# Kernel tuning notes

Measured on AMD Instinct MI355X. Metric: run time of the kernel, lower is better.

Reference implementation:

```python
import jax, jax.numpy as jnp
import numpy as np

N_NODES = 100000
N_EDGES = 1600000
N_GRAPHS = 64
F = 50
N_LAYERS = 3
EPS_STD = 1e-5
EPS_BN = 1e-5


def _glorot(key, shape):
    fan_in, fan_out = shape[0], shape[1]
    lim = float(np.sqrt(6.0 / (fan_in + fan_out)))
    return jax.random.uniform(key, shape, jnp.float32, -lim, lim)


def setup_inputs() -> dict:
    key = jax.random.key(0)
    ks = jax.random.split(key, 20)
    x = jax.random.normal(ks[0], (N_NODES, 2), jnp.float32)
    edge_index = jax.random.randint(ks[1], (2, N_EDGES), 0, N_NODES, jnp.int32)
    batch_ids = jnp.sort(jax.random.randint(ks[2], (N_NODES,), 0, N_GRAPHS, jnp.int32))
    inp = {
        "x": x,
        "edge_index": edge_index,
        "batch_ids": batch_ids,
        "W_gcn": _glorot(ks[3], (2, F)),
        "b_gcn": jnp.zeros((F,), jnp.float32),
        # stacked per-layer PNA params [L, ...]
        "pre_W": jnp.stack([_glorot(jax.random.fold_in(ks[4], i), (2 * F, F)) for i in range(N_LAYERS)]),
        "pre_b": jnp.zeros((N_LAYERS, F), jnp.float32),
        "post_W": jnp.stack([_glorot(jax.random.fold_in(ks[5], i), (13 * F, F)) for i in range(N_LAYERS)]),
        "post_b": jnp.zeros((N_LAYERS, F), jnp.float32),
        "lin_W": jnp.stack([_glorot(jax.random.fold_in(ks[6], i), (F, F)) for i in range(N_LAYERS)]),
        "lin_b": jnp.zeros((N_LAYERS, F), jnp.float32),
        "bn_gamma": jnp.ones((N_LAYERS, F), jnp.float32),
        "bn_beta": jnp.zeros((N_LAYERS, F), jnp.float32),
        "mlp_W1": _glorot(ks[7], (F, 25)),
        "mlp_b1": jnp.zeros((25,), jnp.float32),
        "mlp_W2": _glorot(ks[8], (25, 1)),
        "mlp_b2": jnp.zeros((1,), jnp.float32),
    }
    return inp


def _pna_layer(x, src, dst, deg_raw, deg_c, avg_log, Wp, bp, Wq, bq, Wl, bl):
    # pre-NN on messages: concat(x_i, x_j) -> F   (i = target/dst, j = source/src)
    h = jnp.concatenate([x[dst], x[src]], axis=-1) @ Wp + bp  # [E, F]
    dc = deg_c[:, None]
    s = jax.ops.segment_sum(h, dst, num_segments=N_NODES)
    mean = s / dc
    mean_sq = jax.ops.segment_sum(h * h, dst, num_segments=N_NODES) / dc
    var = jax.nn.relu(mean_sq - mean * mean)
    std = jnp.sqrt(var + EPS_STD)
    has_edge = (deg_raw > 0)[:, None]
    mn = jnp.where(has_edge, jax.ops.segment_min(h, dst, num_segments=N_NODES), 0.0)
    mx = jnp.where(has_edge, jax.ops.segment_max(h, dst, num_segments=N_NODES), 0.0)
    agg = jnp.concatenate([mean, mn, mx, std], axis=-1)  # [N, 4F]
    amp = (jnp.log1p(deg_c) / avg_log)[:, None]
    att = (avg_log / jnp.log1p(deg_c))[:, None]
    out = jnp.concatenate([agg, agg * amp, agg * att], axis=-1)  # [N, 12F]
    out = jnp.concatenate([x, out], axis=-1) @ Wq + bq  # post-NN: [N, 13F] -> F
    return out @ Wl + bl


def reference(x, edge_index, batch_ids, W_gcn, b_gcn, pre_W, pre_b, post_W, post_b,
              lin_W, lin_b, bn_gamma, bn_beta, mlp_W1, mlp_b1, mlp_W2, mlp_b2):
    src, dst = edge_index[0], edge_index[1]

    # ---- GCNConv(2 -> 50) with self loops + symmetric normalization ----
    h = x @ W_gcn
    loop = jnp.arange(N_NODES, dtype=src.dtype)
    src_a = jnp.concatenate([src, loop])
    dst_a = jnp.concatenate([dst, loop])
    deg_sl = jax.ops.segment_sum(jnp.ones_like(src_a, jnp.float32), dst_a, num_segments=N_NODES)
    dinv = jnp.where(deg_sl > 0, jax.lax.rsqrt(deg_sl), 0.0)
    norm = (dinv[src_a] * dinv[dst_a])[:, None]
    h = jax.ops.segment_sum(h[src_a] * norm, dst_a, num_segments=N_NODES) + b_gcn

    # ---- degree stats for PNA scalers ----
    deg_raw = jax.ops.segment_sum(jnp.ones_like(src, jnp.float32), dst, num_segments=N_NODES)
    deg_c = jnp.maximum(deg_raw, 1.0)
    avg_log = jnp.mean(jnp.log1p(deg_raw))

    for l in range(N_LAYERS):
        h = _pna_layer(h, src, dst, deg_raw, deg_c, avg_log,
                       pre_W[l], pre_b[l], post_W[l], post_b[l], lin_W[l], lin_b[l])
        mu = jnp.mean(h, axis=0)
        var = jnp.mean((h - mu) ** 2, axis=0)
        h = (h - mu) * jax.lax.rsqrt(var + EPS_BN) * bn_gamma[l] + bn_beta[l]
        h = jax.nn.relu(h)

    # ---- global add pool + MLP (dropout is identity at eval) ----
    g = jax.ops.segment_sum(h, batch_ids, num_segments=N_GRAPHS)  # [G, F]
    g = jax.nn.relu(g @ mlp_W1 + mlp_b1)
    g = g @ mlp_W2 + mlp_b2  # [G, 1]
    return g.reshape(N_GRAPHS)
```

## Files before the change

### kernel.cpp

```cpp
#include <hip/hip_runtime.h>
#include <math.h>

#define NN 100000
#define NE 1600000
#define NG 64
#define FF 50
#define NL 3
#define NBUCK ((NN + 255) / 256)

typedef short bf16x8 __attribute__((ext_vector_type(8)));
typedef float f32x4 __attribute__((ext_vector_type(4)));

__device__ __forceinline__ short f2bf(float f) {
  return __builtin_bit_cast(short, (__bf16)f);
}
__device__ __forceinline__ float bf2f(short s) {
  unsigned int u = ((unsigned int)(unsigned short)s) << 16;
  return __builtin_bit_cast(float, u);
}

__global__ void k_deg(const int* __restrict__ dst, int* __restrict__ deg) {
  int e = blockIdx.x * blockDim.x + threadIdx.x;
  if (e < NE) atomicAdd(&deg[dst[e]], 1);
}

__global__ void k_scan1(const int* __restrict__ deg, int* __restrict__ off, int* __restrict__ parts) {
  __shared__ int sm[1024];
  int i = blockIdx.x * 1024 + threadIdx.x;
  int v = (i < NN) ? deg[i] : 0;
  sm[threadIdx.x] = v;
  __syncthreads();
  for (int ofs = 1; ofs < 1024; ofs <<= 1) {
    int t = (threadIdx.x >= ofs) ? sm[threadIdx.x - ofs] : 0;
    __syncthreads();
    sm[threadIdx.x] += t;
    __syncthreads();
  }
  if (i < NN) off[i] = sm[threadIdx.x] - v;
  if (threadIdx.x == 1023) parts[blockIdx.x] = sm[1023];
}

__global__ void k_scan2(int* __restrict__ parts, int nb) {
  __shared__ int sm[128];
  int v = (threadIdx.x < nb) ? parts[threadIdx.x] : 0;
  sm[threadIdx.x] = v;
  __syncthreads();
  for (int ofs = 1; ofs < 128; ofs <<= 1) {
    int t = (threadIdx.x >= ofs) ? sm[threadIdx.x - ofs] : 0;
    __syncthreads();
    sm[threadIdx.x] += t;
    __syncthreads();
  }
  if (threadIdx.x < nb) parts[threadIdx.x] = sm[threadIdx.x] - v;
}

__global__ void k_scan3(int* __restrict__ off, const int* __restrict__ parts, int* __restrict__ bcur) {
  int i = blockIdx.x * 256 + threadIdx.x;
  if (i < NN) {
    int v = off[i] + parts[i >> 10];
    off[i] = v;
    if ((i & 255) == 0) bcur[i >> 8] = v;
  }
  if (i == 0) off[NN] = NE;
}

__global__ void k_nodeinit(const int* __restrict__ deg, float* __restrict__ dinv,
                           float* __restrict__ lgc, float* __restrict__ scal) {
  int i = blockIdx.x * 256 + threadIdx.x;
  float lp = 0.f;
  if (i < NN) {
    int d = deg[i];
    dinv[i] = rsqrtf((float)(d + 1));
    int dc = d > 1 ? d : 1;
    lgc[i] = log1pf((float)dc);
    lp = log1pf((float)d);
  }
  for (int o = 32; o > 0; o >>= 1) lp += __shfl_down(lp, o);
  __shared__ float red[4];
  int lane = threadIdx.x & 63, w = threadIdx.x >> 6;
  if (lane == 0) red[w] = lp;
  __syncthreads();
  if (threadIdx.x == 0) atomicAdd(scal, red[0] + red[1] + red[2] + red[3]);
}

__global__ __launch_bounds__(256) void k_bucket(const int* __restrict__ src, const int* __restrict__ dst,
                                                int* __restrict__ bcur, unsigned* __restrict__ tmp) {
  __shared__ int hist[NBUCK];
  __shared__ int base[NBUCK];
  int t = threadIdx.x;
  for (int i = t; i < NBUCK; i += 256) hist[i] = 0;
  __syncthreads();
  int e0 = blockIdx.x * 4096;
  int myb[16], myrank[16];
  unsigned mypack[16];
#pragma unroll
  for (int i = 0; i < 16; ++i) {
    int e = e0 + i * 256 + t;
    if (e < NE) {
      int s = src[e], d = dst[e];
      int b = d >> 8;
      myb[i] = b;
      mypack[i] = ((unsigned)(d & 255) << 17) | (unsigned)s;
      myrank[i] = atomicAdd(&hist[b], 1);
    } else myb[i] = -1;
  }
  __syncthreads();
  for (int i = t; i < NBUCK; i += 256)
    base[i] = hist[i] ? atomicAdd(&bcur[i], hist[i]) : 0;
  __syncthreads();
#pragma unroll
  for (int i = 0; i < 16; ++i)
    if (myb[i] >= 0) tmp[base[myb[i]] + myrank[i]] = mypack[i];
}

__global__ __launch_bounds__(256) void k_bsort(const int* __restrict__ off, const unsigned* __restrict__ tmp,
                                               int* __restrict__ ssrc) {
  int b = blockIdx.x;
  int n0 = b * 256;
  int nEnd = n0 + 256 < NN ? n0 + 256 : NN;
  __shared__ int cnt[256];
  __shared__ int nb[256];
  int t = threadIdx.x;
  cnt[t] = 0;
  if (n0 + t < nEnd) nb[t] = off[n0 + t];
  __syncthreads();
  int lo = off[n0], hiE = off[nEnd];
  for (int e = lo + t; e < hiE; e += 256) {
    unsigned p = tmp[e];
    int dloc = p >> 17;
    int s = (int)(p & 0x1FFFFu);
    int pos = nb[dloc] + atomicAdd(&cnt[dloc], 1);
    ssrc[pos] = s;
  }
}

__global__ void k_fusew(const float* __restrict__ postW, const float* __restrict__ postb,
                        const float* __restrict__ linW, const float* __restrict__ linb,
                        float* __restrict__ A, float* __restrict__ bias2) {
  int wid = (blockIdx.x * blockDim.x + threadIdx.x) >> 6;
  int f = threadIdx.x & 63;
  if (wid >= 3 * 651) return;
  int l = wid / 651, r = wid % 651;
  int fc = f < FF ? f : FF - 1;
  const float* lw = linW + l * FF * FF;
  float acc = 0.f;
  if (r < 650) {
    const float* pw = postW + (l * 650 + r) * FF;
    for (int j = 0; j < FF; ++j) acc += pw[j] * lw[j * FF + fc];
    if (f < FF) A[(l * 650 + r) * FF + f] = acc;
  } else {
    const float* pb = postb + l * FF;
    for (int j = 0; j < FF; ++j) acc += pb[j] * lw[j * FF + fc];
    if (f < FF) bias2[l * 64 + f] = acc + linb[l * FF + f];
  }
}

__global__ void k_packA(const float* __restrict__ Af, short* __restrict__ Abt) {
  int t = blockIdx.x * 256 + threadIdx.x;
  if (t >= 3 * 13 * 64 * 64) return;
  int kk = t & 63;
  int f = (t >> 6) & 63;
  int lc = t >> 12;
  int c = lc % 13;
  int l = lc / 13;
  float v = 0.f;
  if (kk < FF && f < FF) v = Af[((size_t)(l * 650 + c * FF + kk)) * FF + f];
  Abt[t] = f2bf(v);
}

__global__ void k_packP(const float* __restrict__ preW, short* __restrict__ Pbt) {
  int t = blockIdx.x * 256 + threadIdx.x;
  if (t >= NL * 2 * 64 * 64) return;
  int kk = t & 63;
  int f = (t >> 6) & 63;
  int ls = t >> 12;
  int s = ls & 1, l = ls >> 1;
  float v = 0.f;
  if (kk < FF && f < FF) v = preW[(size_t)(l * 100 + s * FF + kk) * FF + f];
  Pbt[t] = f2bf(v);
}

__global__ void k_gcnpre(const float* __restrict__ x, const float* __restrict__ Wg,
                         const float* __restrict__ dinv, short* __restrict__ pb) {
  int t = blockIdx.x * 256 + threadIdx.x;
  int n = t >> 6, f = t & 63;
  if (n >= NN) return;
  float v = 0.f;
  if (f < FF) v = (x[2 * n] * Wg[f] + x[2 * n + 1] * Wg[FF + f]) * dinv[n];
  pb[n * 64 + f] = f2bf(v);
}

__global__ void k_gcnagg(const short* __restrict__ pb, const int* __restrict__ off,
                         const int* __restrict__ ssrc, const float* __restrict__ dinv,
                         const float* __restrict__ bg, float* __restrict__ h) {
  int wid = (blockIdx.x * blockDim.x + threadIdx.x) >> 6;
  int lane = threadIdx.x & 63;
  if (wid >= NN) return;
  int n = wid;
  int fc = lane < FF ? lane : FF - 1;
  float acc = bf2f(pb[n * 64 + fc]);
  int lo = off[n], hi = off[n + 1];
  for (int base = lo; base < hi; base += 64) {
    int rem = hi - base;
    int cnt = rem > 64 ? 64 : rem;
    int sidx = (base + lane < hi) ? ssrc[base + lane] : 0;
    int full = cnt & ~7;
    int j = 0;
    for (; j < full; j += 8) {
#pragma unroll
      for (int i = 0; i < 8; ++i) {
        int s = __builtin_amdgcn_readlane(sidx, j + i);
        acc += bf2f(pb[s * 64 + fc]);
      }
    }
    for (; j < cnt; ++j) {
      int s = __builtin_amdgcn_readlane(sidx, j);
      acc += bf2f(pb[s * 64 + fc]);
    }
  }
  if (lane < FF) h[n * FF + lane] = dinv[n] * acc + bg[lane];
}

__global__ __launch_bounds__(256) void k_preM(const float* __restrict__ hin, const float2* __restrict__ ab,
                                              const short* __restrict__ Pbt, const float* __restrict__ preb,
                                              float* __restrict__ cb, short* __restrict__ bbh, int l) {
  __shared__ short Xs[128][72];
  __shared__ short Bs[2][64][72];
  int tid = threadIdx.x;
  int n0 = blockIdx.x * 128;
  int w = tid >> 6, lane = tid & 63;
  int q = lane >> 4, m16 = lane & 15;

  int bf = tid >> 2, bko = (tid & 3) * 16;
  const short* Pl = Pbt + l * 2 * 4096;
  for (int s = 0; s < 2; ++s) {
    const float4* g = (const float4*)(Pl + (s << 12) + (bf << 6) + bko);
    *(float4*)&Bs[s][bf][bko] = g[0];
    *(float4*)&Bs[s][bf][bko + 8] = g[1];
  }
  int nl = tid & 127, kh = (tid >> 7) * 32;
  int n = n0 + nl;
  bool nvalid = n < NN;
  const float* hrow = hin + (size_t)(nvalid ? n : 0) * FF;
#pragma unroll
  for (int j = 0; j < 32; j += 2) {
    int kk = kh + j;
    float2 v = {0.f, 0.f};
    if (nvalid && kk < FF) v = *(const float2*)(hrow + kk);
    if (ab) {
      float2 p0 = ab[kk], p1 = ab[kk + 1];
      v.x = fmaxf(fmaf(v.x, p0.x, p0.y), 0.f);
      v.y = fmaxf(fmaf(v.y, p1.x, p1.y), 0.f);
    }
    Xs[nl][kk] = f2bf(v.x);
    Xs[nl][kk + 1] = f2bf(v.y);
  }
  __syncthreads();

  f32x4 aT[2][4], aB2[2][4];
#pragma unroll
  for (int i = 0; i < 2; ++i)
#pragma unroll
    for (int j = 0; j < 4; ++j) {
      aT[i][j] = (f32x4){0.f, 0.f, 0.f, 0.f};
      aB2[i][j] = (f32x4){0.f, 0.f, 0.f, 0.f};
    }
#pragma unroll
  for (int hh = 0; hh < 2; ++hh) {
    int ko = hh * 32 + q * 8;
    bf16x8 a0 = *(const bf16x8*)&Xs[w * 32 + m16][ko];
    bf16x8 a1 = *(const bf16x8*)&Xs[w * 32 + 16 + m16][ko];
#pragma unroll
    for (int ft = 0; ft < 4; ++ft) {
      bf16x8 b0 = *(const bf16x8*)&Bs[0][ft * 16 + m16][ko];
      bf16x8 b1 = *(const bf16x8*)&Bs[1][ft * 16 + m16][ko];
      aT[0][ft] = __builtin_amdgcn_mfma_f32_16x16x32_bf16(a0, b0, aT[0][ft], 0, 0, 0);
      aT[1][ft] = __builtin_amdgcn_mfma_f32_16x16x32_bf16(a1, b0, aT[1][ft], 0, 0, 0);
      aB2[0][ft] = __builtin_amdgcn_mfma_f32_16x16x32_bf16(a0, b1, aB2[0][ft], 0, 0, 0);
      aB2[1][ft] = __builtin_amdgcn_mfma_f32_16x16x32_bf16(a1, b1, aB2[1][ft], 0, 0, 0);
    }
  }
#pragma unroll
  for (int mt = 0; mt < 2; ++mt) {
#pragma unroll
    for (int r = 0; r < 4; ++r) {
      int node = n0 + w * 32 + mt * 16 + q * 4 + r;
      if (node >= NN) continue;
#pragma unroll
      for (int ft = 0; ft < 4; ++ft) {
        int col = ft * 16 + m16;
        if (col < FF) cb[node * FF + col] = aT[mt][ft][r] + preb[l * FF + col];
        bbh[node * 64 + col] = f2bf(aB2[mt][ft][r]);
      }
    }
  }
}

__global__ void k_agg(const short* __restrict__ bbh, const float* __restrict__ cb,
                      const int* __restrict__ off, const int* __restrict__ ssrc,
                      const float* __restrict__ lgc, const float* __restrict__ scal,
                      short* __restrict__ agb, float* __restrict__ ampatt) {
  int wid = (blockIdx.x * blockDim.x + threadIdx.x) >> 6;
  int lane = threadIdx.x & 63;
  if (wid >= NN) return;
  int n = wid;
  int fc = lane < FF ? lane : FF - 1;
  float S = 0.f, S2 = 0.f, MN = INFINITY, MX = -INFINITY;
  int lo = off[n], hi = off[n + 1];
  for (int base = lo; base < hi; base += 64) {
    int rem = hi - base;
    int cnt = rem > 64 ? 64 : rem;
    int sidx = (base + lane < hi) ? ssrc[base + lane] : 0;
    int full = cnt & ~7;
    int j = 0;
    for (; j < full; j += 8) {
#pragma unroll
      for (int i = 0; i < 8; ++i) {
        int s = __builtin_amdgcn_readlane(sidx, j + i);
        float v = bf2f(bbh[s * 64 + fc]);
        S += v; S2 = fmaf(v, v, S2);
        MN = fminf(MN, v); MX = fmaxf(MX, v);
      }
    }
    for (; j < cnt; ++j) {
      int s = __builtin_amdgcn_readlane(sidx, j);
      float v = bf2f(bbh[s * 64 + fc]);
      S += v; S2 = fmaf(v, v, S2);
      MN = fminf(MN, v); MX = fmaxf(MX, v);
    }
  }
  int d = hi - lo;
  float mean, mnv, mxv, stdv;
  if (d > 0) {
    float inv = 1.f / (float)d;
    float m = S * inv;
    float var = S2 * inv - m * m; var = var > 0.f ? var : 0.f;
    stdv = sqrtf(var + 1e-5f);
    float c = cb[n * FF + fc];
    mean = c + m; mnv = c + MN; mxv = c + MX;
  } else {
    mean = 0.f; mnv = 0.f; mxv = 0.f; stdv = sqrtf(1e-5f);
  }
  short* row = agb + (size_t)n * 256;
  if (lane < FF) {
    row[lane] = f2bf(mean);
    row[64 + lane] = f2bf(mnv);
    row[128 + lane] = f2bf(mxv);
    row[192 + lane] = f2bf(stdv);
  } else {
    row[lane] = 0; row[64 + lane] = 0; row[128 + lane] = 0; row[192 + lane] = 0;
  }
  if (lane == 0) {
    float avg = scal[0] * (1.f / NN);
    float lg = lgc[n];
    ampatt[2 * n] = lg / avg;
    ampatt[2 * n + 1] = avg / lg;
  }
}

__global__ __launch_bounds__(256) void k_gemm(const float* __restrict__ h, const float2* __restrict__ ab,
                                              const short* __restrict__ agb, const float* __restrict__ ampatt,
                                              const short* __restrict__ Abt, const float* __restrict__ bias2,
                                              float* __restrict__ out, float* __restrict__ bnsum) {
  __shared__ short Xs[128][72];
  __shared__ short Bs[3][64][72];
  __shared__ float2 redbn[4][16][16];
  int tid = threadIdx.x;
  int n0 = blockIdx.x * 128;
  int w = tid >> 6, lane = tid & 63;
  int q = lane >> 4, m16 = lane & 15;

  int nl = tid & 127;
  int kh = (tid >> 7) * 32;
  int n = n0 + nl;
  bool nvalid = n < NN;
  const float* hrow = h + (size_t)(nvalid ? n : 0) * FF;
  const short* arow = agb + (size_t)(nvalid ? n : 0) * 256;

  int bf = tid >> 2;
  int bko = (tid & 3) * 16;

  f32x4 aB[2][4], aC[2][4], aD[2][4];
#pragma unroll
  for (int i = 0; i < 2; ++i)
#pragma unroll
    for (int j = 0; j < 4; ++j) {
      aB[i][j] = (f32x4){0.f, 0.f, 0.f, 0.f};
      aC[i][j] = (f32x4){0.f, 0.f, 0.f, 0.f};
      aD[i][j] = (f32x4){0.f, 0.f, 0.f, 0.f};
    }

  for (int c = 0; c < 5; ++c) {
    if (c) __syncthreads();
    int nslice = (c == 0) ? 1 : 3;
    for (int s = 0; s < nslice; ++s) {
      int chunk = (c == 0) ? 0 : (c + 4 * s);
      const float4* g = (const float4*)(Abt + (chunk << 12) + (bf << 6) + bko);
      *(float4*)&Bs[s][bf][bko] = g[0];
      *(float4*)&Bs[s][bf][bko + 8] = g[1];
    }
    if (c == 0) {
#pragma unroll
      for (int j = 0; j < 32; j += 2) {
        int kk = kh + j;
        float2 v = {0.f, 0.f};
        if (nvalid && kk < FF) v = *(const float2*)(hrow + kk);
        if (ab) {
          float2 p0 = ab[kk], p1 = ab[kk + 1];
          v.x = fmaxf(fmaf(v.x, p0.x, p0.y), 0.f);
          v.y = fmaxf(fmaf(v.y, p1.x, p1.y), 0.f);
        }
        Xs[nl][kk] = f2bf(v.x);
        Xs[nl][kk + 1] = f2bf(v.y);
      }
    } else {
      float4 v0 = {0,0,0,0}, v1 = {0,0,0,0}, v2 = {0,0,0,0}, v3 = {0,0,0,0};
      if (nvalid) {
        const float4* g = (const float4*)(arow + (c - 1) * 64 + kh);
        v0 = g[0]; v1 = g[1]; v2 = g[2]; v3 = g[3];
      }
      float4* dstp = (float4*)&Xs[nl][kh];
      dstp[0] = v0; dstp[1] = v1; dstp[2] = v2; dstp[3] = v3;
    }
    __syncthreads();
#pragma unroll
    for (int hh = 0; hh < 2; ++hh) {
      int ko = hh * 32 + q * 8;
      bf16x8 a0 = *(const bf16x8*)&Xs[w * 32 + m16][ko];
      bf16x8 a1 = *(const bf16x8*)&Xs[w * 32 + 16 + m16][ko];
      if (c == 0) {
#pragma unroll
        for (int ft = 0; ft < 4; ++ft) {
          bf16x8 b = *(const bf16x8*)&Bs[0][ft * 16 + m16][ko];
          aB[0][ft] = __builtin_amdgcn_mfma_f32_16x16x32_bf16(a0, b, aB[0][ft], 0, 0, 0);
          aB[1][ft] = __builtin_amdgcn_mfma_f32_16x16x32_bf16(a1, b, aB[1][ft], 0, 0, 0);
        }
      } else {
#pragma unroll
        for (int ft = 0; ft < 4; ++ft) {
          bf16x8 b0 = *(const bf16x8*)&Bs[0][ft * 16 + m16][ko];
          bf16x8 b1 = *(const bf16x8*)&Bs[1][ft * 16 + m16][ko];
          bf16x8 b2 = *(const bf16x8*)&Bs[2][ft * 16 + m16][ko];
          aB[0][ft] = __builtin_amdgcn_mfma_f32_16x16x32_bf16(a0, b0, aB[0][ft], 0, 0, 0);
          aB[1][ft] = __builtin_amdgcn_mfma_f32_16x16x32_bf16(a1, b0, aB[1][ft], 0, 0, 0);
          aC[0][ft] = __builtin_amdgcn_mfma_f32_16x16x32_bf16(a0, b1, aC[0][ft], 0, 0, 0);
          aC[1][ft] = __builtin_amdgcn_mfma_f32_16x16x32_bf16(a1, b1, aC[1][ft], 0, 0, 0);
          aD[0][ft] = __builtin_amdgcn_mfma_f32_16x16x32_bf16(a0, b2, aD[0][ft], 0, 0, 0);
          aD[1][ft] = __builtin_amdgcn_mfma_f32_16x16x32_bf16(a1, b2, aD[1][ft], 0, 0, 0);
        }
      }
    }
  }
  float sacc[4] = {0.f, 0.f, 0.f, 0.f};
  float qacc[4] = {0.f, 0.f, 0.f, 0.f};
#pragma unroll
  for (int mt = 0; mt < 2; ++mt) {
#pragma unroll
    for (int r = 0; r < 4; ++r) {
      int node = n0 + w * 32 + mt * 16 + q * 4 + r;
      if (node >= NN) continue;
      float2 aa = *(const float2*)(ampatt + 2 * node);
#pragma unroll
      for (int ft = 0; ft < 4; ++ft) {
        int col = ft * 16 + m16;
        if (col >= FF) continue;
        float val = aB[mt][ft][r] + aa.x * aC[mt][ft][r] + aa.y * aD[mt][ft][r] + bias2[col];
        out[node * FF + col] = val;
        sacc[ft] += val;
        qacc[ft] = fmaf(val, val, qacc[ft]);
      }
    }
  }
#pragma unroll
  for (int ft = 0; ft < 4; ++ft)
    redbn[ft][m16][w * 4 + q] = make_float2(sacc[ft], qacc[ft]);
  __syncthreads();
  if (tid < 64) {
    int ftl = tid >> 4, m = tid & 15;
    int col = ftl * 16 + m;
    if (col < FF) {
      float ts = 0.f, tq = 0.f;
#pragma unroll
      for (int i = 0; i < 16; ++i) {
        float2 v = redbn[ftl][m][i];
        ts += v.x; tq += v.y;
      }
      atomicAdd(&bnsum[col], ts);
      atomicAdd(&bnsum[64 + col], tq);
    }
  }
}

__global__ void k_bnab(const float* __restrict__ bnsum, const float* __restrict__ gamma,
                       const float* __restrict__ beta, float2* __restrict__ ab, int l) {
  int f = threadIdx.x;
  float a = 0.f, b = 0.f;
  if (f < FF) {
    float mu = bnsum[f] * (1.f / NN);
    float vq = bnsum[64 + f] * (1.f / NN) - mu * mu;
    float rs = rsqrtf((vq > 0.f ? vq : 0.f) + 1e-5f);
    a = rs * gamma[l * FF + f];
    b = beta[l * FF + f] - mu * a;
  }
  ab[f] = make_float2(a, b);
}

__global__ void k_gsum(const float* __restrict__ h, const float2* __restrict__ ab,
                       const int* __restrict__ batch, float* __restrict__ gsum) {
  int w = threadIdx.x >> 6, lane = threadIdx.x & 63;
  int fc = lane < FF ? lane : FF - 1;
  bool act = lane < FF;
  float2 p = ab[fc];
  int n0 = blockIdx.x * 256 + w * 64;
  if (n0 >= NN) return;
  int nEnd = n0 + 64 < NN ? n0 + 64 : NN;
  float acc = 0.f;
  int gcur = batch[n0];
  for (int n = n0; n < nEnd; ++n) {
    int g = batch[n];
    if (g != gcur) {
      if (act) atomicAdd(&gsum[gcur * 64 + lane], acc);
      acc = 0.f; gcur = g;
    }
    float v = h[n * FF + fc];
    acc += fmaxf(fmaf(v, p.x, p.y), 0.f);
  }
  if (act) atomicAdd(&gsum[gcur * 64 + lane], acc);
}

__global__ void k_mlp(const float* __restrict__ gsum, const float* __restrict__ W1,
                      const float* __restrict__ b1, const float* __restrict__ W2,
                      const float* __restrict__ b2, float* __restrict__ out) {
  int g = threadIdx.x;
  if (g >= NG) return;
  float gv[FF];
#pragma unroll
  for (int f = 0; f < FF; ++f) gv[f] = gsum[g * 64 + f];
  float r = b2[0];
  for (int j = 0; j < 25; ++j) {
    float a = b1[j];
#pragma unroll
    for (int f = 0; f < FF; ++f) a = fmaf(gv[f], W1[f * 25 + j], a);
    r += fmaxf(a, 0.f) * W2[j];
  }
  out[g] = r;
}

extern "C" void kernel_launch(void* const* d_in, const int* in_sizes, int n_in,
                              void* d_out, int out_size, void* d_ws, size_t ws_size,
                              hipStream_t stream) {
  const float* x     = (const float*)d_in[0];
  const int*   ei    = (const int*)d_in[1];
  const int*   src   = ei;
  const int*   dst   = ei + NE;
  const int*   batch = (const int*)d_in[2];
  const float* Wg    = (const float*)d_in[3];
  const float* bg    = (const float*)d_in[4];
  const float* preW  = (const float*)d_in[5];
  const float* preb  = (const float*)d_in[6];
  const float* postW = (const float*)d_in[7];
  const float* postb = (const float*)d_in[8];
  const float* linW  = (const float*)d_in[9];
  const float* linb  = (const float*)d_in[10];
  const float* gamma = (const float*)d_in[11];
  const float* beta  = (const float*)d_in[12];
  const float* W1    = (const float*)d_in[13];
  const float* b1    = (const float*)d_in[14];
  const float* W2    = (const float*)d_in[15];
  const float* b2    = (const float*)d_in[16];
  float* out = (float*)d_out;

  char* W = (char*)d_ws;
  int*    deg    = (int*)(W + 0);
  int*    off    = (int*)(W + 400384);
  int*    bcur   = (int*)(W + 801280);
  int*    parts  = (int*)(W + 803328);
  float*  dinv   = (float*)(W + 807424);
  float*  lgc    = (float*)(W + 1207808);
  float*  scal   = (float*)(W + 1608192);
  float*  bnsum  = (float*)(W + 1608704);
  float2* ab     = (float2*)(W + 1610752);
  float*  Af     = (float*)(W + 1612288);
  float*  bias2  = (float*)(W + 2002432);
  short*  Abt    = (short*)(W + 2003456);
  short*  Pbt    = (short*)(W + 2322944);
  unsigned* tmp  = (unsigned*)(W + 2372096);
  int*    ssrc   = (int*)(W + 8772096);
  float*  hA     = (float*)(W + 15172096);
  float*  hB     = (float*)(W + 35172352);
  float*  cb     = (float*)(W + 55172608);
  short*  bbh    = (short*)(W + 75172864);
  short*  agb    = (short*)(W + 87973120);
  float*  ampatt = (float*)(W + 139173376);
  float*  gsum   = (float*)(W + 139973632);

  hipMemsetAsync(deg, 0, 400384, stream);
  hipMemsetAsync(scal, 0, 2560, stream);
  hipMemsetAsync(gsum, 0, 16384, stream);

  k_deg<<<(NE + 255) / 256, 256, 0, stream>>>(dst, deg);
  k_scan1<<<98, 1024, 0, stream>>>(deg, off, parts);
  k_scan2<<<1, 128, 0, stream>>>(parts, 98);
  k_scan3<<<(NN + 255) / 256, 256, 0, stream>>>(off, parts, bcur);
  k_nodeinit<<<(NN + 255) / 256, 256, 0, stream>>>(deg, dinv, lgc, scal);
  k_bucket<<<(NE + 4095) / 4096, 256, 0, stream>>>(src, dst, bcur, tmp);
  k_bsort<<<NBUCK, 256, 0, stream>>>(off, tmp, ssrc);
  k_fusew<<<(3 * 651 + 3) / 4, 256, 0, stream>>>(postW, postb, linW, linb, Af, bias2);
  k_packA<<<(3 * 13 * 64 * 64 + 255) / 256, 256, 0, stream>>>(Af, Abt);
  k_packP<<<(NL * 2 * 64 * 64 + 255) / 256, 256, 0, stream>>>(preW, Pbt);

  k_gcnpre<<<NN / 4, 256, 0, stream>>>(x, Wg, dinv, bbh);
  k_gcnagg<<<NN / 4, 256, 0, stream>>>(bbh, off, ssrc, dinv, bg, hA);

  float* hin = hA;
  float* hout = hB;
  for (int l = 0; l < NL; ++l) {
    const float2* abl = (l == 0) ? nullptr : (ab + (l - 1) * 64);
    k_preM<<<(NN + 127) / 128, 256, 0, stream>>>(hin, abl, Pbt, preb, cb, bbh, l);
    k_agg<<<NN / 4, 256, 0, stream>>>(bbh, cb, off, ssrc, lgc, scal, agb, ampatt);
    k_gemm<<<(NN + 127) / 128, 256, 0, stream>>>(hin, abl, agb, ampatt, Abt + l * 13 * 4096, bias2 + l * 64, hout, bnsum + l * 128);
    k_bnab<<<1, 64, 0, stream>>>(bnsum + l * 128, gamma, beta, ab + l * 64, l);
    float* t = hin; hin = hout; hout = t;
  }
  k_gsum<<<NBUCK, 256, 0, stream>>>(hin, ab + 2 * 64, batch, gsum);
  k_mlp<<<1, 64, 0, stream>>>(gsum, W1, b1, W2, b2, out);
}
```

Before: 801.1 us.

## Pair-wise bf16 gathers in aggregation, warp-local GEMM tiles, replicated BN atomics

The GCN and PNA aggregation kernels now have each lane load two packed bf16 features per gather, with the two half-waves taking alternate edges and combining at the end through a cross-half shuffle. The preM and post GEMM kernels drop block-level shared B staging and __syncthreads. Each wave now handles its own 16-node tile, reads the weight fragments straight from global memory, and stages the full 320-wide A row in LDS once. BatchNorm partial sums are reduced in-wave and atomically added into 8 replicated slots that k_bnab sums, which is meant to cut sync and atomic contention. The risks are more redundant global weight reads per wave and a workspace layout shift.

New measurement: 936.2 us. +16.9%, slower.

```diff
diff --git a/kernel.cpp b/kernel.cpp
--- a/kernel.cpp
+++ b/kernel.cpp
@@ -17,6 +17,15 @@
 __device__ __forceinline__ float bf2f(short s) {
   unsigned int u = ((unsigned int)(unsigned short)s) << 16;
   return __builtin_bit_cast(float, u);
+}
+__device__ __forceinline__ float2 unpk2(unsigned u) {
+  float2 v;
+  v.x = __builtin_bit_cast(float, u << 16);
+  v.y = __builtin_bit_cast(float, u & 0xFFFF0000u);
+  return v;
+}
+__device__ __forceinline__ unsigned pk2(float2 v) {
+  return (unsigned)(unsigned short)f2bf(v.x) | ((unsigned)(unsigned short)f2bf(v.y) << 16);
 }
 
 __global__ void k_deg(const int* __restrict__ dst, int* __restrict__ deg) {
@@ -197,101 +206,107 @@
   int lane = threadIdx.x & 63;
   if (wid >= NN) return;
   int n = wid;
-  int fc = lane < FF ? lane : FF - 1;
-  float acc = bf2f(pb[n * 64 + fc]);
+  int p = lane & 31;
+  int hf = lane >> 5;
+  float2 acc;
+  {
+    float2 sv = unpk2(*(const unsigned*)(pb + n * 64 + 2 * p));
+    acc.x = hf ? 0.f : sv.x;
+    acc.y = hf ? 0.f : sv.y;
+  }
   int lo = off[n], hi = off[n + 1];
   for (int base = lo; base < hi; base += 64) {
     int rem = hi - base;
     int cnt = rem > 64 ? 64 : rem;
     int sidx = (base + lane < hi) ? ssrc[base + lane] : 0;
-    int full = cnt & ~7;
+    int pairs = cnt >> 1;
     int j = 0;
-    for (; j < full; j += 8) {
-#pragma unroll
-      for (int i = 0; i < 8; ++i) {
-        int s = __builtin_amdgcn_readlane(sidx, j + i);
-        acc += bf2f(pb[s * 64 + fc]);
+    for (; j + 4 <= pairs; j += 4) {
+#pragma unroll
+      for (int i = 0; i < 4; ++i) {
+        int s = __shfl(sidx, 2 * (j + i) + hf);
+        float2 v = unpk2(*(const unsigned*)(pb + s * 64 + 2 * p));
+        acc.x += v.x; acc.y += v.y;
       }
     }
-    for (; j < cnt; ++j) {
-      int s = __builtin_amdgcn_readlane(sidx, j);
-      acc += bf2f(pb[s * 64 + fc]);
-    }
-  }
-  if (lane < FF) h[n * FF + lane] = dinv[n] * acc + bg[lane];
+    for (; j < pairs; ++j) {
+      int s = __shfl(sidx, 2 * j + hf);
+      float2 v = unpk2(*(const unsigned*)(pb + s * 64 + 2 * p));
+      acc.x += v.x; acc.y += v.y;
+    }
+    if (cnt & 1) {
+      int s = __shfl(sidx, cnt - 1);
+      float2 v = unpk2(*(const unsigned*)(pb + s * 64 + 2 * p));
+      if (hf == 0) { acc.x += v.x; acc.y += v.y; }
+    }
+  }
+  acc.x += __shfl_xor(acc.x, 32);
+  acc.y += __shfl_xor(acc.y, 32);
+  if (lane < 32 && p < 25) {
+    float dv = dinv[n];
+    float2 bgp = *(const float2*)(bg + 2 * p);
+    *(float2*)(h + n * FF + 2 * p) = make_float2(dv * acc.x + bgp.x, dv * acc.y + bgp.y);
+  }
 }
 
 __global__ __launch_bounds__(256) void k_preM(const float* __restrict__ hin, const float2* __restrict__ ab,
                                               const short* __restrict__ Pbt, const float* __restrict__ preb,
                                               float* __restrict__ cb, short* __restrict__ bbh, int l) {
-  __shared__ short Xs[128][72];
-  __shared__ short Bs[2][64][72];
+  __shared__ short Xs[64][72];
   int tid = threadIdx.x;
-  int n0 = blockIdx.x * 128;
   int w = tid >> 6, lane = tid & 63;
   int q = lane >> 4, m16 = lane & 15;
-
-  int bf = tid >> 2, bko = (tid & 3) * 16;
-  const short* Pl = Pbt + l * 2 * 4096;
-  for (int s = 0; s < 2; ++s) {
-    const float4* g = (const float4*)(Pl + (s << 12) + (bf << 6) + bko);
-    *(float4*)&Bs[s][bf][bko] = g[0];
-    *(float4*)&Bs[s][bf][bko + 8] = g[1];
-  }
-  int nl = tid & 127, kh = (tid >> 7) * 32;
+  int n0 = blockIdx.x * 64 + w * 16;
+
+  int nl = lane >> 2, ks = lane & 3;
   int n = n0 + nl;
-  bool nvalid = n < NN;
-  const float* hrow = hin + (size_t)(nvalid ? n : 0) * FF;
-#pragma unroll
-  for (int j = 0; j < 32; j += 2) {
-    int kk = kh + j;
-    float2 v = {0.f, 0.f};
-    if (nvalid && kk < FF) v = *(const float2*)(hrow + kk);
-    if (ab) {
-      float2 p0 = ab[kk], p1 = ab[kk + 1];
-      v.x = fmaxf(fmaf(v.x, p0.x, p0.y), 0.f);
-      v.y = fmaxf(fmaf(v.y, p1.x, p1.y), 0.f);
-    }
-    Xs[nl][kk] = f2bf(v.x);
-    Xs[nl][kk + 1] = f2bf(v.y);
-  }
-  __syncthreads();
-
-  f32x4 aT[2][4], aB2[2][4];
-#pragma unroll
-  for (int i = 0; i < 2; ++i)
-#pragma unroll
-    for (int j = 0; j < 4; ++j) {
-      aT[i][j] = (f32x4){0.f, 0.f, 0.f, 0.f};
-      aB2[i][j] = (f32x4){0.f, 0.f, 0.f, 0.f};
-    }
+  bool nv = n < NN;
+  int row = w * 16 + nl;
+  {
+    const float* hrow = hin + (size_t)(nv ? n : 0) * FF;
+    short tmp[16] __attribute__((aligned(16)));
+#pragma unroll
+    for (int j = 0; j < 16; j += 2) {
+      int kk = ks * 16 + j;
+      float2 v = {0.f, 0.f};
+      if (nv && kk < FF) v = *(const float2*)(hrow + kk);
+      if (ab) {
+        float2 p0 = ab[kk], p1 = ab[kk + 1];
+        v.x = fmaxf(fmaf(v.x, p0.x, p0.y), 0.f);
+        v.y = fmaxf(fmaf(v.y, p1.x, p1.y), 0.f);
+      }
+      tmp[j] = f2bf(v.x); tmp[j + 1] = f2bf(v.y);
+    }
+    *(float4*)&Xs[row][ks * 16] = *(const float4*)&tmp[0];
+    *(float4*)&Xs[row][ks * 16 + 8] = *(const float4*)&tmp[8];
+  }
+  const short* P0 = Pbt + l * 8192;
+  f32x4 aT[4], aB2[4];
+#pragma unroll
+  for (int ft = 0; ft < 4; ++ft) {
+    aT[ft] = (f32x4){0.f, 0.f, 0.f, 0.f};
+    aB2[ft] = (f32x4){0.f, 0.f, 0.f, 0.f};
+  }
 #pragma unroll
   for (int hh = 0; hh < 2; ++hh) {
-    int ko = hh * 32 + q * 8;
-    bf16x8 a0 = *(const bf16x8*)&Xs[w * 32 + m16][ko];
-    bf16x8 a1 = *(const bf16x8*)&Xs[w * 32 + 16 + m16][ko];
+    bf16x8 a = *(const bf16x8*)&Xs[w * 16 + m16][hh * 32 + q * 8];
 #pragma unroll
     for (int ft = 0; ft < 4; ++ft) {
-      bf16x8 b0 = *(const bf16x8*)&Bs[0][ft * 16 + m16][ko];
-      bf16x8 b1 = *(const bf16x8*)&Bs[1][ft * 16 + m16][ko];
-      aT[0][ft] = __builtin_amdgcn_mfma_f32_16x16x32_bf16(a0, b0, aT[0][ft], 0, 0, 0);
-      aT[1][ft] = __builtin_amdgcn_mfma_f32_16x16x32_bf16(a1, b0, aT[1][ft], 0, 0, 0);
-      aB2[0][ft] = __builtin_amdgcn_mfma_f32_16x16x32_bf16(a0, b1, aB2[0][ft], 0, 0, 0);
-      aB2[1][ft] = __builtin_amdgcn_mfma_f32_16x16x32_bf16(a1, b1, aB2[1][ft], 0, 0, 0);
-    }
-  }
-#pragma unroll
-  for (int mt = 0; mt < 2; ++mt) {
-#pragma unroll
-    for (int r = 0; r < 4; ++r) {
-      int node = n0 + w * 32 + mt * 16 + q * 4 + r;
-      if (node >= NN) continue;
-#pragma unroll
-      for (int ft = 0; ft < 4; ++ft) {
-        int col = ft * 16 + m16;
-        if (col < FF) cb[node * FF + col] = aT[mt][ft][r] + preb[l * FF + col];
-        bbh[node * 64 + col] = f2bf(aB2[mt][ft][r]);
-      }
+      bf16x8 b0 = *(const bf16x8*)(P0 + ((ft * 16 + m16) << 6) + hh * 32 + q * 8);
+      bf16x8 b1 = *(const bf16x8*)(P0 + 4096 + ((ft * 16 + m16) << 6) + hh * 32 + q * 8);
+      aT[ft] = __builtin_amdgcn_mfma_f32_16x16x32_bf16(a, b0, aT[ft], 0, 0, 0);
+      aB2[ft] = __builtin_amdgcn_mfma_f32_16x16x32_bf16(a, b1, aB2[ft], 0, 0, 0);
+    }
+  }
+#pragma unroll
+  for (int r = 0; r < 4; ++r) {
+    int node = n0 + q * 4 + r;
+    if (node >= NN) continue;
+#pragma unroll
+    for (int ft = 0; ft < 4; ++ft) {
+      int col = ft * 16 + m16;
+      if (col < FF) cb[node * FF + col] = aT[ft][r] + preb[l * FF + col];
+      bbh[node * 64 + col] = f2bf(aB2[ft][r]);
     }
   }
 }
@@ -304,51 +319,75 @@
   int lane = threadIdx.x & 63;
   if (wid >= NN) return;
   int n = wid;
-  int fc = lane < FF ? lane : FF - 1;
-  float S = 0.f, S2 = 0.f, MN = INFINITY, MX = -INFINITY;
+  int p = lane & 31;
+  int hf = lane >> 5;
+  float2 S = {0.f, 0.f}, S2 = {0.f, 0.f};
+  float2 MN = {INFINITY, INFINITY}, MX = {-INFINITY, -INFINITY};
   int lo = off[n], hi = off[n + 1];
   for (int base = lo; base < hi; base += 64) {
     int rem = hi - base;
     int cnt = rem > 64 ? 64 : rem;
     int sidx = (base + lane < hi) ? ssrc[base + lane] : 0;
-    int full = cnt & ~7;
+    int pairs = cnt >> 1;
     int j = 0;
-    for (; j < full; j += 8) {
-#pragma unroll
-      for (int i = 0; i < 8; ++i) {
-        int s = __builtin_amdgcn_readlane(sidx, j + i);
-        float v = bf2f(bbh[s * 64 + fc]);
-        S += v; S2 = fmaf(v, v, S2);
-        MN = fminf(MN, v); MX = fmaxf(MX, v);
+    for (; j + 4 <= pairs; j += 4) {
+#pragma unroll
+      for (int i = 0; i < 4; ++i) {
+        int s = __shfl(sidx, 2 * (j + i) + hf);
+        float2 v = unpk2(*(const unsigned*)(bbh + s * 64 + 2 * p));
+        S.x += v.x; S.y += v.y;
+        S2.x = fmaf(v.x, v.x, S2.x); S2.y = fmaf(v.y, v.y, S2.y);
+        MN.x = fminf(MN.x, v.x); MN.y = fminf(MN.y, v.y);
+        MX.x = fmaxf(MX.x, v.x); MX.y = fmaxf(MX.y, v.y);
       }
     }
-    for (; j < cnt; ++j) {
-      int s = __builtin_amdgcn_readlane(sidx, j);
-      float v = bf2f(bbh[s * 64 + fc]);
-      S += v; S2 = fmaf(v, v, S2);
-      MN = fminf(MN, v); MX = fmaxf(MX, v);
-    }
-  }
+    for (; j < pairs; ++j) {
+      int s = __shfl(sidx, 2 * j + hf);
+      float2 v = unpk2(*(const unsigned*)(bbh + s * 64 + 2 * p));
+      S.x += v.x; S.y += v.y;
+      S2.x = fmaf(v.x, v.x, S2.x); S2.y = fmaf(v.y, v.y, S2.y);
+      MN.x = fminf(MN.x, v.x); MN.y = fminf(MN.y, v.y);
+      MX.x = fmaxf(MX.x, v.x); MX.y = fmaxf(MX.y, v.y);
+    }
+    if (cnt & 1) {
+      int s = __shfl(sidx, cnt - 1);
+      float2 v = unpk2(*(const unsigned*)(bbh + s * 64 + 2 * p));
+      if (hf == 0) {
+        S.x += v.x; S.y += v.y;
+        S2.x = fmaf(v.x, v.x, S2.x); S2.y = fmaf(v.y, v.y, S2.y);
+        MN.x = fminf(MN.x, v.x); MN.y = fminf(MN.y, v.y);
+        MX.x = fmaxf(MX.x, v.x); MX.y = fmaxf(MX.y, v.y);
+      }
+    }
+  }
+  S.x += __shfl_xor(S.x, 32);   S.y += __shfl_xor(S.y, 32);
+  S2.x += __shfl_xor(S2.x, 32); S2.y += __shfl_xor(S2.y, 32);
+  MN.x = fminf(MN.x, __shfl_xor(MN.x, 32)); MN.y = fminf(MN.y, __shfl_xor(MN.y, 32));
+  MX.x = fmaxf(MX.x, __shfl_xor(MX.x, 32)); MX.y = fmaxf(MX.y, __shfl_xor(MX.y, 32));
   int d = hi - lo;
-  float mean, mnv, mxv, stdv;
+  bool valid = p < 25;
+  float2 mean, mnv, mxv, stdv;
   if (d > 0) {
     float inv = 1.f / (float)d;
-    float m = S * inv;
-    float var = S2 * inv - m * m; var = var > 0.f ? var : 0.f;
-    stdv = sqrtf(var + 1e-5f);
-    float c = cb[n * FF + fc];
-    mean = c + m; mnv = c + MN; mxv = c + MX;
+    float2 m = make_float2(S.x * inv, S.y * inv);
+    float vx = S2.x * inv - m.x * m.x; vx = vx > 0.f ? vx : 0.f;
+    float vy = S2.y * inv - m.y * m.y; vy = vy > 0.f ? vy : 0.f;
+    stdv = make_float2(sqrtf(vx + 1e-5f), sqrtf(vy + 1e-5f));
+    float2 c = valid ? *(const float2*)(cb + n * FF + 2 * p) : make_float2(0.f, 0.f);
+    mean = make_float2(c.x + m.x, c.y + m.y);
+    mnv = make_float2(c.x + MN.x, c.y + MN.y);
+    mxv = make_float2(c.x + MX.x, c.y + MX.y);
   } else {
-    mean = 0.f; mnv = 0.f; mxv = 0.f; stdv = sqrtf(1e-5f);
-  }
-  short* row = agb + (size_t)n * 256;
-  if (lane < FF) {
-    row[lane] = f2bf(mean);
-    row[64 + lane] = f2bf(mnv);
-    row[128 + lane] = f2bf(mxv);
-    row[192 + lane] = f2bf(stdv);
-  } else {
-    row[lane] = 0; row[64 + lane] = 0; row[128 + lane] = 0; row[192 + lane] = 0;
+    mean = mnv = mxv = make_float2(0.f, 0.f);
+    float sq = sqrtf(1e-5f);
+    stdv = make_float2(sq, sq);
+  }
+  if (lane < 32) {
+    unsigned* row32 = (unsigned*)(agb + (size_t)n * 256);
+    row32[p]      = valid ? pk2(mean) : 0u;
+    row32[32 + p] = valid ? pk2(mnv) : 0u;
+    row32[64 + p] = valid ? pk2(mxv) : 0u;
+    row32[96 + p] = valid ? pk2(stdv) : 0u;
   }
   if (lane == 0) {
     float avg = scal[0] * (1.f / NN);
@@ -358,95 +397,75 @@
   }
 }
 
-__global__ __launch_bounds__(256) void k_gemm(const float* __restrict__ h, const float2* __restrict__ ab,
-                                              const short* __restrict__ agb, const float* __restrict__ ampatt,
-                                              const short* __restrict__ Abt, const float* __restrict__ bias2,
-                                              float* __restrict__ out, float* __restrict__ bnsum) {
-  __shared__ short Xs[128][72];
-  __shared__ short Bs[3][64][72];
-  __shared__ float2 redbn[4][16][16];
+__global__ __launch_bounds__(256, 3) void k_gemm(const float* __restrict__ h, const float2* __restrict__ ab,
+                                                 const short* __restrict__ agb, const float* __restrict__ ampatt,
+                                                 const short* __restrict__ Abt, const float* __restrict__ bias2,
+                                                 float* __restrict__ out, float* __restrict__ bnsumR) {
+  __shared__ short Xs[64][328];
   int tid = threadIdx.x;
-  int n0 = blockIdx.x * 128;
   int w = tid >> 6, lane = tid & 63;
   int q = lane >> 4, m16 = lane & 15;
-
-  int nl = tid & 127;
-  int kh = (tid >> 7) * 32;
+  int n0 = blockIdx.x * 64 + w * 16;
+
+  int nl = lane >> 2, ks = lane & 3;
   int n = n0 + nl;
-  bool nvalid = n < NN;
-  const float* hrow = h + (size_t)(nvalid ? n : 0) * FF;
-  const short* arow = agb + (size_t)(nvalid ? n : 0) * 256;
-
-  int bf = tid >> 2;
-  int bko = (tid & 3) * 16;
-
-  f32x4 aB[2][4], aC[2][4], aD[2][4];
-#pragma unroll
-  for (int i = 0; i < 2; ++i)
-#pragma unroll
-    for (int j = 0; j < 4; ++j) {
-      aB[i][j] = (f32x4){0.f, 0.f, 0.f, 0.f};
-      aC[i][j] = (f32x4){0.f, 0.f, 0.f, 0.f};
-      aD[i][j] = (f32x4){0.f, 0.f, 0.f, 0.f};
-    }
-
-  for (int c = 0; c < 5; ++c) {
-    if (c) __syncthreads();
-    int nslice = (c == 0) ? 1 : 3;
-    for (int s = 0; s < nslice; ++s) {
-      int chunk = (c == 0) ? 0 : (c + 4 * s);
-      const float4* g = (const float4*)(Abt + (chunk << 12) + (bf << 6) + bko);
-      *(float4*)&Bs[s][bf][bko] = g[0];
-      *(float4*)&Bs[s][bf][bko + 8] = g[1];
-    }
-    if (c == 0) {
-#pragma unroll
-      for (int j = 0; j < 32; j += 2) {
-        int kk = kh + j;
-        float2 v = {0.f, 0.f};
-        if (nvalid && kk < FF) v = *(const float2*)(hrow + kk);
-        if (ab) {
-          float2 p0 = ab[kk], p1 = ab[kk + 1];
-          v.x = fmaxf(fmaf(v.x, p0.x, p0.y), 0.f);
-          v.y = fmaxf(fmaf(v.y, p1.x, p1.y), 0.f);
-        }
-        Xs[nl][kk] = f2bf(v.x);
-        Xs[nl][kk + 1] = f2bf(v.y);
+  bool nv = n < NN;
+  int row = w * 16 + nl;
+  const short* arow = agb + (size_t)(nv ? n : 0) * 256;
+#pragma unroll
+  for (int c = 1; c <= 4; ++c) {
+    const float4* g = (const float4*)(arow + (c - 1) * 64 + ks * 16);
+    float4 z = {0.f, 0.f, 0.f, 0.f};
+    float4 v0 = nv ? g[0] : z;
+    float4 v1 = nv ? g[1] : z;
+    *(float4*)&Xs[row][c * 64 + ks * 16] = v0;
+    *(float4*)&Xs[row][c * 64 + ks * 16 + 8] = v1;
+  }
+  {
+    const float* hrow = h + (size_t)(nv ? n : 0) * FF;
+    short tmp[16] __attribute__((aligned(16)));
+#pragma unroll
+    for (int j = 0; j < 16; j += 2) {
+      int kk = ks * 16 + j;
+      float2 v = {0.f, 0.f};
+      if (nv && kk < FF) v = *(const float2*)(hrow + kk);
+      if (ab) {
+        float2 p0 = ab[kk], p1 = ab[kk + 1];
+        v.x = fmaxf(fmaf(v.x, p0.x, p0.y), 0.f);
+        v.y = fmaxf(fmaf(v.y, p1.x, p1.y), 0.f);
       }
-    } else {
-      float4 v0 = {0,0,0,0}, v1 = {0,0,0,0}, v2 = {0,0,0,0}, v3 = {0,0,0,0};
-      if (nvalid) {
-        const float4* g = (const float4*)(arow + (c - 1) * 64 + kh);
-        v0 = g[0]; v1 = g[1]; v2 = g[2]; v3 = g[3];
-      }
-      float4* dstp = (float4*)&Xs[nl][kh];
-      dstp[0] = v0; dstp[1] = v1; dstp[2] = v2; dstp[3] = v3;
-    }
-    __syncthreads();
+      tmp[j] = f2bf(v.x); tmp[j + 1] = f2bf(v.y);
+    }
+    *(float4*)&Xs[row][ks * 16] = *(const float4*)&tmp[0];
+    *(float4*)&Xs[row][ks * 16 + 8] = *(const float4*)&tmp[8];
+  }
+
+  f32x4 acc[3][4];
+#pragma unroll
+  for (int s = 0; s < 3; ++s)
+#pragma unroll
+    for (int ft = 0; ft < 4; ++ft) acc[s][ft] = (f32x4){0.f, 0.f, 0.f, 0.f};
+
+#pragma unroll
+  for (int hh = 0; hh < 2; ++hh) {
+    bf16x8 a = *(const bf16x8*)&Xs[w * 16 + m16][hh * 32 + q * 8];
+#pragma unroll
+    for (int ft = 0; ft < 4; ++ft) {
+      bf16x8 b = *(const bf16x8*)(Abt + ((ft * 16 + m16) << 6) + hh * 32 + q * 8);
+      acc[0][ft] = __builtin_amdgcn_mfma_f32_16x16x32_bf16(a, b, acc[0][ft], 0, 0, 0);
+    }
+  }
+  for (int c = 1; c <= 4; ++c) {
 #pragma unroll
     for (int hh = 0; hh < 2; ++hh) {
-      int ko = hh * 32 + q * 8;
-      bf16x8 a0 = *(const bf16x8*)&Xs[w * 32 + m16][ko];
-      bf16x8 a1 = *(const bf16x8*)&Xs[w * 32 + 16 + m16][ko];
-      if (c == 0) {
+      bf16x8 a = *(const bf16x8*)&Xs[w * 16 + m16][c * 64 + hh * 32 + q * 8];
+#pragma unroll
+      for (int s = 0; s < 3; ++s) {
+        const short* Bc = Abt + ((c + 4 * s) << 12);
 #pragma unroll
         for (int ft = 0; ft < 4; ++ft) {
-          bf16x8 b = *(const bf16x8*)&Bs[0][ft * 16 + m16][ko];
-          aB[0][ft] = __builtin_amdgcn_mfma_f32_16x16x32_bf16(a0, b, aB[0][ft], 0, 0, 0);
-          aB[1][ft] = __builtin_amdgcn_mfma_f32_16x16x32_bf16(a1, b, aB[1][ft], 0, 0, 0);
-        }
-      } else {
-#pragma unroll
-        for (int ft = 0; ft < 4; ++ft) {
-          bf16x8 b0 = *(const bf16x8*)&Bs[0][ft * 16 + m16][ko];
-          bf16x8 b1 = *(const bf16x8*)&Bs[1][ft * 16 + m16][ko];
-          bf16x8 b2 = *(const bf16x8*)&Bs[2][ft * 16 + m16][ko];
-          aB[0][ft] = __builtin_amdgcn_mfma_f32_16x16x32_bf16(a0, b0, aB[0][ft], 0, 0, 0);
-          aB[1][ft] = __builtin_amdgcn_mfma_f32_16x16x32_bf16(a1, b0, aB[1][ft], 0, 0, 0);
-          aC[0][ft] = __builtin_amdgcn_mfma_f32_16x16x32_bf16(a0, b1, aC[0][ft], 0, 0, 0);
-          aC[1][ft] = __builtin_amdgcn_mfma_f32_16x16x32_bf16(a1, b1, aC[1][ft], 0, 0, 0);
-          aD[0][ft] = __builtin_amdgcn_mfma_f32_16x16x32_bf16(a0, b2, aD[0][ft], 0, 0, 0);
-          aD[1][ft] = __builtin_amdgcn_mfma_f32_16x16x32_bf16(a1, b2, aD[1][ft], 0, 0, 0);
+          bf16x8 b = *(const bf16x8*)(Bc + ((ft * 16 + m16) << 6) + hh * 32 + q * 8);
+          acc[s][ft] = __builtin_amdgcn_mfma_f32_16x16x32_bf16(a, b, acc[s][ft], 0, 0, 0);
         }
       }
     }
@@ -454,50 +473,49 @@
   float sacc[4] = {0.f, 0.f, 0.f, 0.f};
   float qacc[4] = {0.f, 0.f, 0.f, 0.f};
 #pragma unroll
-  for (int mt = 0; mt < 2; ++mt) {
-#pragma unroll
-    for (int r = 0; r < 4; ++r) {
-      int node = n0 + w * 32 + mt * 16 + q * 4 + r;
-      if (node >= NN) continue;
-      float2 aa = *(const float2*)(ampatt + 2 * node);
-#pragma unroll
-      for (int ft = 0; ft < 4; ++ft) {
-        int col = ft * 16 + m16;
-        if (col >= FF) continue;
-        float val = aB[mt][ft][r] + aa.x * aC[mt][ft][r] + aa.y * aD[mt][ft][r] + bias2[col];
-        out[node * FF + col] = val;
-        sacc[ft] += val;
-        qacc[ft] = fmaf(val, val, qacc[ft]);
+  for (int r = 0; r < 4; ++r) {
+    int node = n0 + q * 4 + r;
+    if (node >= NN) continue;
+    float2 aa = *(const float2*)(ampatt + 2 * node);
+#pragma unroll
+    for (int ft = 0; ft < 4; ++ft) {
+      int col = ft * 16 + m16;
+      if (col >= FF) continue;
+      float val = acc[0][ft][r] + aa.x * acc[1][ft][r] + aa.y * acc[2][ft][r] + bias2[col];
+      out[node * FF + col] = val;
+      sacc[ft] += val;
+      qacc[ft] = fmaf(val, val, qacc[ft]);
+    }
+  }
+#pragma unroll
+  for (int ft = 0; ft < 4; ++ft) {
+    sacc[ft] += __shfl_xor(sacc[ft], 16);
+    sacc[ft] += __shfl_xor(sacc[ft], 32);
+    qacc[ft] += __shfl_xor(qacc[ft], 16);
+    qacc[ft] += __shfl_xor(qacc[ft], 32);
+  }
+  if (lane < 16) {
+    float* bl = bnsumR + (blockIdx.x & 7) * 128;
+#pragma unroll
+    for (int ft = 0; ft < 4; ++ft) {
+      int col = ft * 16 + lane;
+      if (col < FF) {
+        atomicAdd(&bl[col], sacc[ft]);
+        atomicAdd(&bl[64 + col], qacc[ft]);
       }
     }
   }
-#pragma unroll
-  for (int ft = 0; ft < 4; ++ft)
-    redbn[ft][m16][w * 4 + q] = make_float2(sacc[ft], qacc[ft]);
-  __syncthreads();
-  if (tid < 64) {
-    int ftl = tid >> 4, m = tid & 15;
-    int col = ftl * 16 + m;
-    if (col < FF) {
-      float ts = 0.f, tq = 0.f;
-#pragma unroll
-      for (int i = 0; i < 16; ++i) {
-        float2 v = redbn[ftl][m][i];
-        ts += v.x; tq += v.y;
-      }
-      atomicAdd(&bnsum[col], ts);
-      atomicAdd(&bnsum[64 + col], tq);
-    }
-  }
-}
-
-__global__ void k_bnab(const float* __restrict__ bnsum, const float* __restrict__ gamma,
+}
+
+__global__ void k_bnab(const float* __restrict__ bnsumR, const float* __restrict__ gamma,
                        const float* __restrict__ beta, float2* __restrict__ ab, int l) {
   int f = threadIdx.x;
   float a = 0.f, b = 0.f;
   if (f < FF) {
-    float mu = bnsum[f] * (1.f / NN);
-    float vq = bnsum[64 + f] * (1.f / NN) - mu * mu;
+    float s = 0.f, q = 0.f;
+    for (int r = 0; r < 8; ++r) { s += bnsumR[r * 128 + f]; q += bnsumR[r * 128 + 64 + f]; }
+    float mu = s * (1.f / NN);
+    float vq = q * (1.f / NN) - mu * mu;
     float rs = rsqrtf((vq > 0.f ? vq : 0.f) + 1e-5f);
     a = rs * gamma[l * FF + f];
     b = beta[l * FF + f] - mu * a;
@@ -579,23 +597,23 @@
   float*  lgc    = (float*)(W + 1207808);
   float*  scal   = (float*)(W + 1608192);
   float*  bnsum  = (float*)(W + 1608704);
-  float2* ab     = (float2*)(W + 1610752);
-  float*  Af     = (float*)(W + 1612288);
-  float*  bias2  = (float*)(W + 2002432);
-  short*  Abt    = (short*)(W + 2003456);
-  short*  Pbt    = (short*)(W + 2322944);
-  unsigned* tmp  = (unsigned*)(W + 2372096);
-  int*    ssrc   = (int*)(W + 8772096);
-  float*  hA     = (float*)(W + 15172096);
-  float*  hB     = (float*)(W + 35172352);
-  float*  cb     = (float*)(W + 55172608);
-  short*  bbh    = (short*)(W + 75172864);
-  short*  agb    = (short*)(W + 87973120);
-  float*  ampatt = (float*)(W + 139173376);
-  float*  gsum   = (float*)(W + 139973632);
+  float2* ab     = (float2*)(W + 1620992);
+  float*  Af     = (float*)(W + 1622528);
+  float*  bias2  = (float*)(W + 2012672);
+  short*  Abt    = (short*)(W + 2013696);
+  short*  Pbt    = (short*)(W + 2333184);
+  unsigned* tmp  = (unsigned*)(W + 2382336);
+  int*    ssrc   = (int*)(W + 8782336);
+  float*  hA     = (float*)(W + 15182336);
+  float*  hB     = (float*)(W + 35182592);
+  float*  cb     = (float*)(W + 55182848);
+  short*  bbh    = (short*)(W + 75183104);
+  short*  agb    = (short*)(W + 87983360);
+  float*  ampatt = (float*)(W + 139183616);
+  float*  gsum   = (float*)(W + 139983872);
 
   hipMemsetAsync(deg, 0, 400384, stream);
-  hipMemsetAsync(scal, 0, 2560, stream);
+  hipMemsetAsync(scal, 0, 12800, stream);
   hipMemsetAsync(gsum, 0, 16384, stream);
 
   k_deg<<<(NE + 255) / 256, 256, 0, stream>>>(dst, deg);
@@ -616,10 +634,12 @@
   float* hout = hB;
   for (int l = 0; l < NL; ++l) {
     const float2* abl = (l == 0) ? nullptr : (ab + (l - 1) * 64);
-    k_preM<<<(NN + 127) / 128, 256, 0, stream>>>(hin, abl, Pbt, preb, cb, bbh, l);
+    k_preM<<<(NN + 63) / 64, 256, 0, stream>>>(hin, abl, Pbt, preb, cb, bbh, l);
     k_agg<<<NN / 4, 256, 0, stream>>>(bbh, cb, off, ssrc, lgc, scal, agb, ampatt);
-    k_gemm<<<(NN + 127) / 128, 256, 0, stream>>>(hin, abl, agb, ampatt, Abt + l * 13 * 4096, bias2 + l * 64, hout, bnsum + l * 128);
-    k_bnab<<<1, 64, 0, stream>>>(bnsum + l * 128, gamma, beta, ab + l * 64, l);
+    k_gemm<<<(NN + 63) / 64, 256, 0, stream>>>(hin, abl, agb, ampatt,
+                                               Abt + l * 13 * 4096, bias2 + l * 64, hout,
+                                               bnsum + l * 1024);
+    k_bnab<<<1, 64, 0, stream>>>(bnsum + l * 1024, gamma, beta, ab + l * 64, l);
     float* t = hin; hin = hout; hout = t;
   }
   k_gsum<<<NBUCK, 256, 0, stream>>>(hin, ab + 2 * 64, batch, gsum);
```
